# Kernel optimization log

Hardware: AMD Instinct MI355X
Metric: run time of the kernel (lower is better)

## Reference

```python
import jax, jax.numpy as jnp
import numpy as np

N, IN_DIM, HID, Z, HEADS, E = 10000, 128, 128, 64, 4, 320000
NEG_SLOPE = 0.2


def setup_inputs() -> dict:
    key = jax.random.key(0)
    ks = jax.random.split(key, 16)
    s = 0.1
    return {
        "x": jax.random.normal(ks[0], (N, IN_DIM), jnp.float32),
        "edge_index": jax.random.randint(ks[1], (2, E), 0, N, jnp.int64),
        "gcn_w": jax.random.normal(ks[2], (IN_DIM, HID), jnp.float32) * s,
        "gcn_b": jnp.zeros((HID,), jnp.float32),
        "gat_w": jax.random.normal(ks[3], (HID, HEADS * HID), jnp.float32) * s,
        "gat_att_src": jax.random.normal(ks[4], (HEADS, HID), jnp.float32) * s,
        "gat_att_dst": jax.random.normal(ks[5], (HEADS, HID), jnp.float32) * s,
        "gat_b": jnp.zeros((HID,), jnp.float32),
        "mlp_w1": jax.random.normal(ks[6], (HID, HID), jnp.float32) * s,
        "mlp_b1": jnp.zeros((HID,), jnp.float32),
        "mlp_w2": jax.random.normal(ks[7], (HID, HID), jnp.float32) * s,
        "mlp_b2": jnp.zeros((HID,), jnp.float32),
        "mu_w": jax.random.normal(ks[8], (HID, Z), jnp.float32) * s,
        "mu_b": jnp.zeros((Z,), jnp.float32),
        "lv_w": jax.random.normal(ks[9], (HID, Z), jnp.float32) * s,
        "lv_b": jnp.zeros((Z,), jnp.float32),
    }


def _add_self_loops(edge_index, n):
    loop = jnp.arange(n, dtype=edge_index.dtype)
    src = jnp.concatenate([edge_index[0], loop])
    dst = jnp.concatenate([edge_index[1], loop])
    return src, dst


def _gcn(x, edge_index, w, b):
    # PyG GCNConv: add self-loops, symmetric normalization D^-1/2 (A+I) D^-1/2
    n = x.shape[0]
    src, dst = _add_self_loops(edge_index, n)
    deg = jax.ops.segment_sum(jnp.ones_like(dst, dtype=x.dtype), dst, num_segments=n)
    dinv = jax.lax.rsqrt(deg)  # deg >= 1 due to self-loops
    norm = dinv[src] * dinv[dst]  # [E+N]
    h = x @ w  # [N, HID]
    out = jax.ops.segment_sum(h[src] * norm[:, None], dst, num_segments=n)
    return out + b


def _gat(x, edge_index, w, att_src, att_dst, b):
    # PyG GATConv(heads=HEADS, concat=False): average heads, self-loops added
    n = x.shape[0]
    src, dst = _add_self_loops(edge_index, n)
    h = (x @ w).reshape(n, HEADS, HID)  # [N, H, C]
    a_src = jnp.einsum('nhc,hc->nh', h, att_src)  # [N, H]
    a_dst = jnp.einsum('nhc,hc->nh', h, att_dst)
    e = jax.nn.leaky_relu(a_src[src] + a_dst[dst], NEG_SLOPE)  # [E+N, H]
    # segment softmax over incoming edges of each destination node
    emax = jax.ops.segment_max(e, dst, num_segments=n)
    e = jnp.exp(e - emax[dst])
    denom = jax.ops.segment_sum(e, dst, num_segments=n)
    alpha = e / denom[dst]  # [E+N, H]
    out = jax.ops.segment_sum(h[src] * alpha[:, :, None], dst, num_segments=n)  # [N, H, C]
    return out.mean(axis=1) + b


def reference(x, edge_index, gcn_w, gcn_b, gat_w, gat_att_src, gat_att_dst, gat_b,
              mlp_w1, mlp_b1, mlp_w2, mlp_b2, mu_w, mu_b, lv_w, lv_b):
    h = jax.nn.relu(_gcn(x, edge_index, gcn_w, gcn_b))
    h = jax.nn.relu(_gat(h, edge_index, gat_w, gat_att_src, gat_att_dst, gat_b))
    h = jax.nn.relu(h @ mlp_w1 + mlp_b1)
    h = jax.nn.relu(h @ mlp_w2 + mlp_b2)
    mu = h @ mu_w + mu_b
    logvar = h @ lv_w + lv_b
    return (mu, logvar)
```

## Files before the change

kernel.cpp:

```cpp
#include <hip/hip_runtime.h>

#define NN 10000
#define D 128
#define NH 4
#define HD 512
#define ZD 64

__device__ __forceinline__ float lrelu(float x){ return x > 0.0f ? x : 0.2f*x; }

__global__ __launch_bounds__(256) void k_zero_int(int* __restrict__ a, int n){
  int i = blockIdx.x*256 + threadIdx.x;
  if (i < n) a[i] = 0;
}

__global__ __launch_bounds__(256) void k_hist(const int* __restrict__ dst,
                                              int* __restrict__ deg, int E){
  int i = blockIdx.x*256 + threadIdx.x;
  if (i < E) atomicAdd(&deg[dst[i]], 1);
}

__global__ __launch_bounds__(1024) void k_scan(int* __restrict__ deg,
                                               int* __restrict__ ioff,
                                               float* __restrict__ dinv){
  __shared__ int part[1024];
  const int tid = threadIdx.x;
  const int base = tid*10;
  int local[10]; int s = 0;
#pragma unroll
  for (int i=0;i<10;i++){
    int idx = base+i;
    int v = (idx < NN) ? deg[idx] : 0;
    if (idx < NN) dinv[idx] = rsqrtf(1.0f + (float)v);
    local[i] = s; s += v;
  }
  part[tid] = s;
  __syncthreads();
  for (int o=1;o<1024;o<<=1){
    int v = (tid>=o) ? part[tid-o] : 0;
    __syncthreads();
    part[tid] += v;
    __syncthreads();
  }
  int excl = part[tid] - s;
#pragma unroll
  for (int i=0;i<10;i++){
    int idx = base+i;
    if (idx < NN){
      int o = excl + local[i];
      ioff[idx] = o;
      deg[idx]  = o;
    }
  }
  if (tid == 1023) ioff[NN] = part[1023];
}

__global__ __launch_bounds__(256) void k_fill(const int* __restrict__ src,
                                              const int* __restrict__ dst,
                                              int* __restrict__ cur,
                                              int* __restrict__ csr, int E,
                                              float* __restrict__ az){
  int i = blockIdx.x*256 + threadIdx.x;
  if (i < NN*NH*2) az[i] = 0.f;
  if (i >= E) return;
  int pos = atomicAdd(&cur[dst[i]], 1);
  csr[pos] = src[i];
}

__global__ __launch_bounds__(256) void k_gemm(const float* __restrict__ A,
                                              const float* __restrict__ W, int ldw,
                                              const float* __restrict__ bias,
                                              float* __restrict__ C, int ldc,
                                              int nrows, int do_relu){
  __shared__ float As[64][132];
  __shared__ float Ws[128][68];
  const int tid  = threadIdx.x;
  const int row0 = blockIdx.x*64;
  const int col0 = blockIdx.y*64;
#pragma unroll
  for (int i=0;i<8;i++){
    int f  = tid + i*256;
    int r  = f >> 5;
    int k4 = (f & 31) << 2;
    int rr = row0 + r;
    float4 v = make_float4(0.f,0.f,0.f,0.f);
    if (rr < nrows) v = *(const float4*)&A[rr*D + k4];
    *(float4*)&As[r][k4] = v;
  }
#pragma unroll
  for (int i=0;i<8;i++){
    int f  = tid + i*256;
    int k  = f >> 4;
    int c4 = (f & 15) << 2;
    float4 v = *(const float4*)&W[k*ldw + col0 + c4];
    *(float4*)&Ws[k][c4] = v;
  }
  __syncthreads();
  const int tx = tid & 15, ty = tid >> 4;
  float acc[4][4] = {{0.f}};
#pragma unroll 4
  for (int k=0;k<128;k++){
    float4 w = *(const float4*)&Ws[k][tx<<2];
    float wv[4] = {w.x, w.y, w.z, w.w};
    float av[4];
#pragma unroll
    for (int i=0;i<4;i++) av[i] = As[(ty<<2)+i][k];
#pragma unroll
    for (int i=0;i<4;i++)
#pragma unroll
      for (int j=0;j<4;j++) acc[i][j] = fmaf(av[i], wv[j], acc[i][j]);
  }
#pragma unroll
  for (int i=0;i<4;i++){
    int r = row0 + (ty<<2) + i;
    if (r >= nrows) continue;
#pragma unroll
    for (int j=0;j<4;j++){
      int c = col0 + (tx<<2) + j;
      float v = acc[i][j];
      if (bias) v += bias[c];
      if (do_relu) v = fmaxf(v, 0.f);
      C[r*ldc + c] = v;
    }
  }
}

__global__ __launch_bounds__(128) void k_watt(const float* __restrict__ gat_w,
                                              const float* __restrict__ att_src,
                                              const float* __restrict__ att_dst,
                                              float* __restrict__ w_as,
                                              float* __restrict__ w_ad){
  const int h = blockIdx.x;
  const int k = threadIdx.x;
  const float* wrow = &gat_w[k*HD + h*D];
  const float* as   = &att_src[h*D];
  const float* ad   = &att_dst[h*D];
  float s = 0.f, d = 0.f;
#pragma unroll 4
  for (int c=0;c<D;c++){
    float wv = wrow[c];
    s = fmaf(wv, as[c], s);
    d = fmaf(wv, ad[c], d);
  }
  w_as[h*D + k] = s;
  w_ad[h*D + k] = d;
}

__global__ __launch_bounds__(256) void k_gcn_agg(const float* __restrict__ xw,
                                                 const float* __restrict__ dinv,
                                                 const int* __restrict__ ioff,
                                                 const int* __restrict__ csr,
                                                 const float* __restrict__ bias,
                                                 const float* __restrict__ w_as,
                                                 const float* __restrict__ w_ad,
                                                 float* __restrict__ out,
                                                 float* __restrict__ a_src,
                                                 float* __restrict__ a_dst){
  __shared__ float2 snm[4][64];
  const int sub  = blockIdx.x & 7;
  const int ch   = sub >> 2;
  const int g    = blockIdx.x >> 3;
  const int wv   = threadIdx.x >> 6;
  const int lane = threadIdx.x & 63;
  const int w    = g*16 + (sub & 3)*4 + wv;
  const int c    = ch*64 + lane;
  const int beg = ioff[w], end = ioff[w+1];
  float din = dinv[w];
  float ax = xw[w*D + c] * din;
  for (int jb = beg; jb < end; jb += 64){
    int cnt = end - jb; if (cnt > 64) cnt = 64;
    if (lane < cnt){
      int s = csr[jb + lane];
      snm[wv][lane] = make_float2(dinv[s], __int_as_float(s));
    }
    __builtin_amdgcn_wave_barrier();
#pragma unroll 4
    for (int l=0; l<cnt; l++){
      float2 t = snm[wv][l];
      int ss = __float_as_int(t.y);
      ax = fmaf(t.x, xw[ss*D + c], ax);
    }
    __builtin_amdgcn_wave_barrier();
  }
  float val = fmaxf(fmaf(ax, din, bias[c]), 0.f);
  out[w*D + c] = val;
  float ps[NH], pd[NH];
#pragma unroll
  for (int h=0;h<NH;h++){
    ps[h] = val * w_as[h*D + c];
    pd[h] = val * w_ad[h*D + c];
  }
#pragma unroll
  for (int o=32;o>0;o>>=1){
#pragma unroll
    for (int h=0;h<NH;h++){
      ps[h] += __shfl_xor(ps[h], o);
      pd[h] += __shfl_xor(pd[h], o);
    }
  }
  if (lane == 0){
#pragma unroll
    for (int h=0;h<NH;h++){
      atomicAdd(&a_src[w*4 + h], ps[h]);
      atomicAdd(&a_dst[w*4 + h], pd[h]);
    }
  }
}

__global__ __launch_bounds__(256) void k_gat_agg2(const float* __restrict__ h1,
                                                  const float* __restrict__ a_src,
                                                  const float* __restrict__ a_dst,
                                                  const int* __restrict__ ioff,
                                                  const int* __restrict__ csr,
                                                  float* __restrict__ agg){
  __shared__ float4 sal[4][64];
  __shared__ int    ssr[4][64];
  const int sub  = blockIdx.x & 7;
  const int ch   = sub >> 2;
  const int g    = blockIdx.x >> 3;
  const int wv   = threadIdx.x >> 6;
  const int lane = threadIdx.x & 63;
  const int w    = g*16 + (sub & 3)*4 + wv;
  const int c    = ch*64 + lane;
  const int beg = ioff[w], end = ioff[w+1];
  float4 ad  = *(const float4*)&a_dst[w*4];
  float4 asn = *(const float4*)&a_src[w*4];
  float e0 = __expf(lrelu(asn.x + ad.x));
  float e1 = __expf(lrelu(asn.y + ad.y));
  float e2 = __expf(lrelu(asn.z + ad.z));
  float e3 = __expf(lrelu(asn.w + ad.w));
  float hv = h1[w*D + c];
  float o0 = e0*hv, o1 = e1*hv, o2 = e2*hv, o3 = e3*hv;
  float den0=0.f, den1=0.f, den2=0.f, den3=0.f;

  for (int jb = beg; jb < end; jb += 64){
    int cnt = end - jb; if (cnt > 64) cnt = 64;
    if (lane < cnt){
      int s = csr[jb + lane];
      float4 as = *(const float4*)&a_src[s*4];
      float g0 = __expf(lrelu(as.x + ad.x));
      float g1 = __expf(lrelu(as.y + ad.y));
      float g2 = __expf(lrelu(as.z + ad.z));
      float g3 = __expf(lrelu(as.w + ad.w));
      sal[wv][lane] = make_float4(g0,g1,g2,g3);
      ssr[wv][lane] = s;
      den0 += g0; den1 += g1; den2 += g2; den3 += g3;
    }
    __builtin_amdgcn_wave_barrier();
#pragma unroll 4
    for (int l=0; l<cnt; l++){
      float4 b = sal[wv][l];
      float sv = h1[ssr[wv][l]*D + c];
      o0 = fmaf(b.x, sv, o0);
      o1 = fmaf(b.y, sv, o1);
      o2 = fmaf(b.z, sv, o2);
      o3 = fmaf(b.w, sv, o3);
    }
    __builtin_amdgcn_wave_barrier();
  }
#pragma unroll
  for (int o=32; o>0; o>>=1){
    den0 += __shfl_xor(den0, o);
    den1 += __shfl_xor(den1, o);
    den2 += __shfl_xor(den2, o);
    den3 += __shfl_xor(den3, o);
  }
  den0 += e0; den1 += e1; den2 += e2; den3 += e3;
  float* ab = &agg[(size_t)w*HD + c];
  ab[0*D] = o0 * (0.25f/den0);
  ab[1*D] = o1 * (0.25f/den1);
  ab[2*D] = o2 * (0.25f/den2);
  ab[3*D] = o3 * (0.25f/den3);
}

__global__ __launch_bounds__(256) void k_gemm2(const float* __restrict__ agg,
                                               const float* __restrict__ W,
                                               const float* __restrict__ bias,
                                               float* __restrict__ h2){
  __shared__ float As[64][132];
  __shared__ float Ws[128][68];
  const int tid  = threadIdx.x;
  const int row0 = blockIdx.x*64;
  const int col0 = blockIdx.y*64;
  const int tx = tid & 15, ty = tid >> 4;
  float acc[4][4] = {{0.f}};
  for (int h=0; h<NH; h++){
    __syncthreads();
#pragma unroll
    for (int i=0;i<8;i++){
      int f  = tid + i*256;
      int r  = f >> 5;
      int k4 = (f & 31) << 2;
      int rr = row0 + r;
      float4 v = make_float4(0.f,0.f,0.f,0.f);
      if (rr < NN) v = *(const float4*)&agg[(size_t)rr*HD + h*D + k4];
      *(float4*)&As[r][k4] = v;
    }
#pragma unroll
    for (int i=0;i<8;i++){
      int f  = tid + i*256;
      int k  = f >> 4;
      int c4 = (f & 15) << 2;
      *(float4*)&Ws[k][c4] = *(const float4*)&W[k*HD + h*D + col0 + c4];
    }
    __syncthreads();
#pragma unroll 4
    for (int k=0;k<128;k++){
      float4 w = *(const float4*)&Ws[k][tx<<2];
      float wv[4] = {w.x, w.y, w.z, w.w};
      float av[4];
#pragma unroll
      for (int i=0;i<4;i++) av[i] = As[(ty<<2)+i][k];
#pragma unroll
      for (int i=0;i<4;i++)
#pragma unroll
        for (int j=0;j<4;j++) acc[i][j] = fmaf(av[i], wv[j], acc[i][j]);
    }
  }
#pragma unroll
  for (int i=0;i<4;i++){
    int r = row0 + (ty<<2) + i;
    if (r >= NN) continue;
#pragma unroll
    for (int j=0;j<4;j++){
      int col = col0 + (tx<<2) + j;
      h2[r*D + col] = fmaxf(acc[i][j] + bias[col], 0.f);
    }
  }
}

__global__ __launch_bounds__(256) void k_mlp(const float* __restrict__ h2,
                                             const float* __restrict__ w1,
                                             const float* __restrict__ b1,
                                             const float* __restrict__ w2,
                                             const float* __restrict__ b2,
                                             const float* __restrict__ wmu,
                                             const float* __restrict__ bmu,
                                             const float* __restrict__ wlv,
                                             const float* __restrict__ blv,
                                             float* __restrict__ out){
  __shared__ float hA[32][132];
  __shared__ float hB[32][132];
  __shared__ float Ws[128][68];
  const int tid  = threadIdx.x;
  const int row0 = blockIdx.x*32;
  const int tx = tid & 15, ty = tid >> 4;

#pragma unroll
  for (int i=0;i<4;i++){
    int f  = tid + i*256;
    int r  = f >> 5;
    int k4 = (f & 31) << 2;
    int rr = row0 + r;
    float4 v = make_float4(0.f,0.f,0.f,0.f);
    if (rr < NN) v = *(const float4*)&h2[rr*D + k4];
    *(float4*)&hA[r][k4] = v;
  }

  float (*S)[132] = hA;
  float (*T)[132] = hB;
#pragma unroll
  for (int layer=0; layer<2; layer++){
    const float* W  = layer ? w2 : w1;
    const float* bb = layer ? b2 : b1;
    for (int cc=0; cc<2; cc++){
      __syncthreads();
#pragma unroll
      for (int i=0;i<8;i++){
        int f  = tid + i*256;
        int k  = f >> 4;
        int c4 = (f & 15) << 2;
        *(float4*)&Ws[k][c4] = *(const float4*)&W[k*D + cc*64 + c4];
      }
      __syncthreads();
      float acc[2][4] = {{0.f}};
#pragma unroll 4
      for (int k=0;k<128;k++){
        float4 wvv = *(const float4*)&Ws[k][tx<<2];
        float wv[4] = {wvv.x, wvv.y, wvv.z, wvv.w};
        float av[2];
#pragma unroll
        for (int i=0;i<2;i++) av[i] = S[(ty<<1)+i][k];
#pragma unroll
        for (int i=0;i<2;i++)
#pragma unroll
          for (int j=0;j<4;j++) acc[i][j] = fmaf(av[i], wv[j], acc[i][j]);
      }
#pragma unroll
      for (int i=0;i<2;i++)
#pragma unroll
        for (int j=0;j<4;j++){
          int col = cc*64 + (tx<<2) + j;
          T[(ty<<1)+i][col] = fmaxf(acc[i][j] + bb[col], 0.f);
        }
    }
    float (*tmp)[132] = S; S = T; T = tmp;
  }
  for (int cc=0; cc<2; cc++){
    const float* W  = cc ? wlv : wmu;
    const float* bb = cc ? blv : bmu;
    float* ob = out + (size_t)cc*NN*ZD;
    __syncthreads();
#pragma unroll
    for (int i=0;i<8;i++){
      int f  = tid + i*256;
      int k  = f >> 4;
      int c4 = (f & 15) << 2;
      *(float4*)&Ws[k][c4] = *(const float4*)&W[k*ZD + c4];
    }
    __syncthreads();
    float acc[2][4] = {{0.f}};
#pragma unroll 4
    for (int k=0;k<128;k++){
      float4 wvv = *(const float4*)&Ws[k][tx<<2];
      float wv[4] = {wvv.x, wvv.y, wvv.z, wvv.w};
      float av[2];
#pragma unroll
      for (int i=0;i<2;i++) av[i] = S[(ty<<1)+i][k];
#pragma unroll
      for (int i=0;i<2;i++)
#pragma unroll
        for (int j=0;j<4;j++) acc[i][j] = fmaf(av[i], wv[j], acc[i][j]);
    }
#pragma unroll
    for (int i=0;i<2;i++){
      int r = row0 + (ty<<1) + i;
      if (r >= NN) continue;
      float4 v = make_float4(acc[i][0] + bb[(tx<<2)+0],
                             acc[i][1] + bb[(tx<<2)+1],
                             acc[i][2] + bb[(tx<<2)+2],
                             acc[i][3] + bb[(tx<<2)+3]);
      *(float4*)&ob[r*ZD + (tx<<2)] = v;
    }
  }
}

extern "C" void kernel_launch(void* const* d_in, const int* in_sizes, int n_in,
                              void* d_out, int out_size, void* d_ws, size_t ws_size,
                              hipStream_t stream){
  const float* x     = (const float*)d_in[0];
  const int*   ei    = (const int*)d_in[1];
  const float* gcn_w = (const float*)d_in[2];
  const float* gcn_b = (const float*)d_in[3];
  const float* gat_w = (const float*)d_in[4];
  const float* att_s = (const float*)d_in[5];
  const float* att_d = (const float*)d_in[6];
  const float* gat_b = (const float*)d_in[7];
  const float* w1    = (const float*)d_in[8];
  const float* b1    = (const float*)d_in[9];
  const float* w2    = (const float*)d_in[10];
  const float* b2    = (const float*)d_in[11];
  const float* mu_w  = (const float*)d_in[12];
  const float* mu_b  = (const float*)d_in[13];
  const float* lv_w  = (const float*)d_in[14];
  const float* lv_b  = (const float*)d_in[15];
  const int E = in_sizes[1] / 2;
  const int* src = ei;
  const int* dst = ei + E;

  float* ws    = (float*)d_ws;
  float* xw    = ws;
  float* h1    = xw + NN*D;
  float* h2    = h1 + NN*D;
  float* agg   = h2 + NN*D;
  float* dinv  = agg + (size_t)NN*HD;
  float* w_as  = dinv + NN;
  float* w_ad  = w_as + HD;
  float* a_src = w_ad + HD;
  float* a_dst = a_src + NN*NH;
  int*   ioff  = (int*)(a_dst + NN*NH);
  int*   icur  = ioff + NN + 1;
  int*   csr   = icur + NN;

  const int gN = (NN + 255)/256;
  const int gE = (E + 255)/256;
  const int gR = (NN + 63)/64;
  const int gM = (NN + 31)/32;

  k_zero_int<<<gN, 256, 0, stream>>>(icur, NN);
  k_hist<<<gE, 256, 0, stream>>>(dst, icur, E);
  k_scan<<<1, 1024, 0, stream>>>(icur, ioff, dinv);
  k_fill<<<gE, 256, 0, stream>>>(src, dst, icur, csr, E, a_src);

  k_watt<<<NH, 128, 0, stream>>>(gat_w, att_s, att_d, w_as, w_ad);

  k_gemm<<<dim3(gR,2), 256, 0, stream>>>(x, gcn_w, D, nullptr, xw, D, NN, 0);
  k_gcn_agg<<<(NN/16)*8, 256, 0, stream>>>(xw, dinv, ioff, csr, gcn_b,
                                           w_as, w_ad, h1, a_src, a_dst);

  k_gat_agg2<<<(NN/16)*8, 256, 0, stream>>>(h1, a_src, a_dst, ioff, csr, agg);
  k_gemm2<<<dim3(gR,2), 256, 0, stream>>>(agg, gat_w, gat_b, h2);

  k_mlp<<<gM, 256, 0, stream>>>(h2, w1, b1, w2, b2, mu_w, mu_b, lv_w, lv_b,
                                (float*)d_out);
}
```

Baseline: 191.7 us.

## Merge prologue kernels into one launch and fuse GAT projection GEMM into MLP

Combines the zeroing of the degree counters, the attention-weight precompute and the GCN input GEMM into a single multi-role kernel, cutting two launches. The head-summing GAT projection GEMM is folded into the MLP kernel using 32-row tiles, so the h2 intermediate never goes to global memory and one more launch disappears. The trade-off is that the GAT GEMM now runs on smaller tiles with fewer blocks (313) and reloads weights once per block, which lowers per-block data reuse and parallelism for the largest GEMM.

```diff
diff --git a/kernel.cpp b/kernel.cpp
--- a/kernel.cpp
+++ b/kernel.cpp
@@ -7,11 +7,6 @@
 #define ZD 64
 
 __device__ __forceinline__ float lrelu(float x){ return x > 0.0f ? x : 0.2f*x; }
-
-__global__ __launch_bounds__(256) void k_zero_int(int* __restrict__ a, int n){
-  int i = blockIdx.x*256 + threadIdx.x;
-  if (i < n) a[i] = 0;
-}
 
 __global__ __launch_bounds__(256) void k_hist(const int* __restrict__ dst,
                                               int* __restrict__ deg, int E){
@@ -66,83 +61,83 @@
   csr[pos] = src[i];
 }
 
-__global__ __launch_bounds__(256) void k_gemm(const float* __restrict__ A,
-                                              const float* __restrict__ W, int ldw,
-                                              const float* __restrict__ bias,
-                                              float* __restrict__ C, int ldc,
-                                              int nrows, int do_relu){
-  __shared__ float As[64][132];
-  __shared__ float Ws[128][68];
-  const int tid  = threadIdx.x;
-  const int row0 = blockIdx.x*64;
-  const int col0 = blockIdx.y*64;
-#pragma unroll
-  for (int i=0;i<8;i++){
-    int f  = tid + i*256;
-    int r  = f >> 5;
-    int k4 = (f & 31) << 2;
-    int rr = row0 + r;
-    float4 v = make_float4(0.f,0.f,0.f,0.f);
-    if (rr < nrows) v = *(const float4*)&A[rr*D + k4];
-    *(float4*)&As[r][k4] = v;
-  }
-#pragma unroll
-  for (int i=0;i<8;i++){
-    int f  = tid + i*256;
-    int k  = f >> 4;
-    int c4 = (f & 15) << 2;
-    float4 v = *(const float4*)&W[k*ldw + col0 + c4];
-    *(float4*)&Ws[k][c4] = v;
-  }
-  __syncthreads();
-  const int tx = tid & 15, ty = tid >> 4;
-  float acc[4][4] = {{0.f}};
-#pragma unroll 4
-  for (int k=0;k<128;k++){
-    float4 w = *(const float4*)&Ws[k][tx<<2];
-    float wv[4] = {w.x, w.y, w.z, w.w};
-    float av[4];
-#pragma unroll
-    for (int i=0;i<4;i++) av[i] = As[(ty<<2)+i][k];
-#pragma unroll
-    for (int i=0;i<4;i++)
-#pragma unroll
-      for (int j=0;j<4;j++) acc[i][j] = fmaf(av[i], wv[j], acc[i][j]);
-  }
-#pragma unroll
-  for (int i=0;i<4;i++){
-    int r = row0 + (ty<<2) + i;
-    if (r >= nrows) continue;
-#pragma unroll
-    for (int j=0;j<4;j++){
-      int c = col0 + (tx<<2) + j;
-      float v = acc[i][j];
-      if (bias) v += bias[c];
-      if (do_relu) v = fmaxf(v, 0.f);
-      C[r*ldc + c] = v;
-    }
-  }
-}
-
-__global__ __launch_bounds__(128) void k_watt(const float* __restrict__ gat_w,
+__global__ __launch_bounds__(256) void k_mega(const float* __restrict__ x,
+                                              const float* __restrict__ gcn_w,
+                                              float* __restrict__ xw,
+                                              const float* __restrict__ gat_w,
                                               const float* __restrict__ att_src,
                                               const float* __restrict__ att_dst,
                                               float* __restrict__ w_as,
-                                              float* __restrict__ w_ad){
-  const int h = blockIdx.x;
-  const int k = threadIdx.x;
-  const float* wrow = &gat_w[k*HD + h*D];
-  const float* as   = &att_src[h*D];
-  const float* ad   = &att_dst[h*D];
-  float s = 0.f, d = 0.f;
+                                              float* __restrict__ w_ad,
+                                              int* __restrict__ icur){
+  __shared__ float As[64][132];
+  __shared__ float Ws[128][68];
+  const int bx  = blockIdx.x;
+  const int tid = threadIdx.x;
+  if (bx < 314){
+    const int row0 = (bx >> 1)*64;
+    const int col0 = (bx & 1)*64;
+#pragma unroll
+    for (int i=0;i<8;i++){
+      int f  = tid + i*256;
+      int r  = f >> 5;
+      int k4 = (f & 31) << 2;
+      int rr = row0 + r;
+      float4 v = make_float4(0.f,0.f,0.f,0.f);
+      if (rr < NN) v = *(const float4*)&x[rr*D + k4];
+      *(float4*)&As[r][k4] = v;
+    }
+#pragma unroll
+    for (int i=0;i<8;i++){
+      int f  = tid + i*256;
+      int k  = f >> 4;
+      int c4 = (f & 15) << 2;
+      *(float4*)&Ws[k][c4] = *(const float4*)&gcn_w[k*D + col0 + c4];
+    }
+    __syncthreads();
+    const int tx = tid & 15, ty = tid >> 4;
+    float acc[4][4] = {{0.f}};
 #pragma unroll 4
-  for (int c=0;c<D;c++){
-    float wv = wrow[c];
-    s = fmaf(wv, as[c], s);
-    d = fmaf(wv, ad[c], d);
-  }
-  w_as[h*D + k] = s;
-  w_ad[h*D + k] = d;
+    for (int k=0;k<128;k++){
+      float4 w = *(const float4*)&Ws[k][tx<<2];
+      float wv[4] = {w.x, w.y, w.z, w.w};
+      float av[4];
+#pragma unroll
+      for (int i=0;i<4;i++) av[i] = As[(ty<<2)+i][k];
+#pragma unroll
+      for (int i=0;i<4;i++)
+#pragma unroll
+        for (int j=0;j<4;j++) acc[i][j] = fmaf(av[i], wv[j], acc[i][j]);
+    }
+#pragma unroll
+    for (int i=0;i<4;i++){
+      int r = row0 + (ty<<2) + i;
+      if (r >= NN) continue;
+#pragma unroll
+      for (int j=0;j<4;j++)
+        xw[r*D + col0 + (tx<<2) + j] = acc[i][j];
+    }
+  } else if (bx < 318){
+    const int h = bx - 314;
+    const int k = tid;
+    if (k < 128){
+      const float* wrow = &gat_w[k*HD + h*D];
+      const float* as   = &att_src[h*D];
+      const float* ad   = &att_dst[h*D];
+      float s = 0.f, d = 0.f;
+#pragma unroll 4
+      for (int c=0;c<D;c++){
+        float wv = wrow[c];
+        s = fmaf(wv, as[c], s);
+        d = fmaf(wv, ad[c], d);
+      }
+      w_as[h*D + k] = s;
+      w_ad[h*D + k] = d;
+    }
+  } else {
+    int i = (bx - 318)*256 + tid;
+    if (i < NN) icur[i] = 0;
+  }
 }
 
 __global__ __launch_bounds__(256) void k_gcn_agg(const float* __restrict__ xw,
@@ -272,133 +267,131 @@
   ab[3*D] = o3 * (0.25f/den3);
 }
 
-__global__ __launch_bounds__(256) void k_gemm2(const float* __restrict__ agg,
-                                               const float* __restrict__ W,
-                                               const float* __restrict__ bias,
-                                               float* __restrict__ h2){
-  __shared__ float As[64][132];
+#define KLOOP(ACC)                                            \
+  _Pragma("unroll 4")                                         \
+  for (int k=0;k<128;k++){                                    \
+    float4 wvv = *(const float4*)&Ws[k][tx<<2];               \
+    float av0 = S[(ty<<1)+0][k];                              \
+    float av1 = S[(ty<<1)+1][k];                              \
+    ACC[0][0] = fmaf(av0, wvv.x, ACC[0][0]);                  \
+    ACC[0][1] = fmaf(av0, wvv.y, ACC[0][1]);                  \
+    ACC[0][2] = fmaf(av0, wvv.z, ACC[0][2]);                  \
+    ACC[0][3] = fmaf(av0, wvv.w, ACC[0][3]);                  \
+    ACC[1][0] = fmaf(av1, wvv.x, ACC[1][0]);                  \
+    ACC[1][1] = fmaf(av1, wvv.y, ACC[1][1]);                  \
+    ACC[1][2] = fmaf(av1, wvv.z, ACC[1][2]);                  \
+    ACC[1][3] = fmaf(av1, wvv.w, ACC[1][3]);                  \
+  }
+
+__global__ __launch_bounds__(256) void k_gat_mlp(const float* __restrict__ agg,
+                                                 const float* __restrict__ gat_w,
+                                                 const float* __restrict__ gat_b,
+                                                 const float* __restrict__ w1,
+                                                 const float* __restrict__ b1,
+                                                 const float* __restrict__ w2,
+                                                 const float* __restrict__ b2,
+                                                 const float* __restrict__ wmu,
+                                                 const float* __restrict__ bmu,
+                                                 const float* __restrict__ wlv,
+                                                 const float* __restrict__ blv,
+                                                 float* __restrict__ out){
+  __shared__ float S[32][132];
   __shared__ float Ws[128][68];
   const int tid  = threadIdx.x;
-  const int row0 = blockIdx.x*64;
-  const int col0 = blockIdx.y*64;
+  const int row0 = blockIdx.x*32;
   const int tx = tid & 15, ty = tid >> 4;
-  float acc[4][4] = {{0.f}};
+  float accA[2][4] = {{0.f}};
+  float accB[2][4] = {{0.f}};
+
   for (int h=0; h<NH; h++){
     __syncthreads();
 #pragma unroll
-    for (int i=0;i<8;i++){
+    for (int i=0;i<4;i++){
       int f  = tid + i*256;
       int r  = f >> 5;
       int k4 = (f & 31) << 2;
       int rr = row0 + r;
       float4 v = make_float4(0.f,0.f,0.f,0.f);
       if (rr < NN) v = *(const float4*)&agg[(size_t)rr*HD + h*D + k4];
-      *(float4*)&As[r][k4] = v;
-    }
-#pragma unroll
-    for (int i=0;i<8;i++){
-      int f  = tid + i*256;
-      int k  = f >> 4;
-      int c4 = (f & 15) << 2;
-      *(float4*)&Ws[k][c4] = *(const float4*)&W[k*HD + h*D + col0 + c4];
-    }
-    __syncthreads();
-#pragma unroll 4
-    for (int k=0;k<128;k++){
-      float4 w = *(const float4*)&Ws[k][tx<<2];
-      float wv[4] = {w.x, w.y, w.z, w.w};
-      float av[4];
-#pragma unroll
-      for (int i=0;i<4;i++) av[i] = As[(ty<<2)+i][k];
-#pragma unroll
-      for (int i=0;i<4;i++)
-#pragma unroll
-        for (int j=0;j<4;j++) acc[i][j] = fmaf(av[i], wv[j], acc[i][j]);
-    }
-  }
-#pragma unroll
-  for (int i=0;i<4;i++){
-    int r = row0 + (ty<<2) + i;
-    if (r >= NN) continue;
+      *(float4*)&S[r][k4] = v;
+    }
+    __syncthreads();
+#pragma unroll
+    for (int i=0;i<8;i++){
+      int f  = tid + i*256;
+      int k  = f >> 4;
+      int c4 = (f & 15) << 2;
+      *(float4*)&Ws[k][c4] = *(const float4*)&gat_w[k*HD + h*D + 0 + c4];
+    }
+    __syncthreads();
+    KLOOP(accA)
+    __syncthreads();
+#pragma unroll
+    for (int i=0;i<8;i++){
+      int f  = tid + i*256;
+      int k  = f >> 4;
+      int c4 = (f & 15) << 2;
+      *(float4*)&Ws[k][c4] = *(const float4*)&gat_w[k*HD + h*D + 64 + c4];
+    }
+    __syncthreads();
+    KLOOP(accB)
+  }
+  __syncthreads();
+#pragma unroll
+  for (int i=0;i<2;i++)
 #pragma unroll
     for (int j=0;j<4;j++){
-      int col = col0 + (tx<<2) + j;
-      h2[r*D + col] = fmaxf(acc[i][j] + bias[col], 0.f);
-    }
-  }
-}
-
-__global__ __launch_bounds__(256) void k_mlp(const float* __restrict__ h2,
-                                             const float* __restrict__ w1,
-                                             const float* __restrict__ b1,
-                                             const float* __restrict__ w2,
-                                             const float* __restrict__ b2,
-                                             const float* __restrict__ wmu,
-                                             const float* __restrict__ bmu,
-                                             const float* __restrict__ wlv,
-                                             const float* __restrict__ blv,
-                                             float* __restrict__ out){
-  __shared__ float hA[32][132];
-  __shared__ float hB[32][132];
-  __shared__ float Ws[128][68];
-  const int tid  = threadIdx.x;
-  const int row0 = blockIdx.x*32;
-  const int tx = tid & 15, ty = tid >> 4;
-
-#pragma unroll
-  for (int i=0;i<4;i++){
-    int f  = tid + i*256;
-    int r  = f >> 5;
-    int k4 = (f & 31) << 2;
-    int rr = row0 + r;
-    float4 v = make_float4(0.f,0.f,0.f,0.f);
-    if (rr < NN) v = *(const float4*)&h2[rr*D + k4];
-    *(float4*)&hA[r][k4] = v;
-  }
-
-  float (*S)[132] = hA;
-  float (*T)[132] = hB;
-#pragma unroll
+      int c0 = (tx<<2) + j;
+      S[(ty<<1)+i][c0]      = fmaxf(accA[i][j] + gat_b[c0],      0.f);
+      S[(ty<<1)+i][c0 + 64] = fmaxf(accB[i][j] + gat_b[c0 + 64], 0.f);
+    }
+
   for (int layer=0; layer<2; layer++){
     const float* W  = layer ? w2 : w1;
     const float* bb = layer ? b2 : b1;
-    for (int cc=0; cc<2; cc++){
-      __syncthreads();
-#pragma unroll
-      for (int i=0;i<8;i++){
-        int f  = tid + i*256;
-        int k  = f >> 4;
-        int c4 = (f & 15) << 2;
-        *(float4*)&Ws[k][c4] = *(const float4*)&W[k*D + cc*64 + c4];
+#pragma unroll
+    for (int i=0;i<2;i++)
+#pragma unroll
+      for (int j=0;j<4;j++){ accA[i][j] = 0.f; accB[i][j] = 0.f; }
+    __syncthreads();
+#pragma unroll
+    for (int i=0;i<8;i++){
+      int f  = tid + i*256;
+      int k  = f >> 4;
+      int c4 = (f & 15) << 2;
+      *(float4*)&Ws[k][c4] = *(const float4*)&W[k*D + 0 + c4];
+    }
+    __syncthreads();
+    KLOOP(accA)
+    __syncthreads();
+#pragma unroll
+    for (int i=0;i<8;i++){
+      int f  = tid + i*256;
+      int k  = f >> 4;
+      int c4 = (f & 15) << 2;
+      *(float4*)&Ws[k][c4] = *(const float4*)&W[k*D + 64 + c4];
+    }
+    __syncthreads();
+    KLOOP(accB)
+    __syncthreads();
+#pragma unroll
+    for (int i=0;i<2;i++)
+#pragma unroll
+      for (int j=0;j<4;j++){
+        int c0 = (tx<<2) + j;
+        S[(ty<<1)+i][c0]      = fmaxf(accA[i][j] + bb[c0],      0.f);
+        S[(ty<<1)+i][c0 + 64] = fmaxf(accB[i][j] + bb[c0 + 64], 0.f);
       }
-      __syncthreads();
-      float acc[2][4] = {{0.f}};
-#pragma unroll 4
-      for (int k=0;k<128;k++){
-        float4 wvv = *(const float4*)&Ws[k][tx<<2];
-        float wv[4] = {wvv.x, wvv.y, wvv.z, wvv.w};
-        float av[2];
-#pragma unroll
-        for (int i=0;i<2;i++) av[i] = S[(ty<<1)+i][k];
-#pragma unroll
-        for (int i=0;i<2;i++)
-#pragma unroll
-          for (int j=0;j<4;j++) acc[i][j] = fmaf(av[i], wv[j], acc[i][j]);
-      }
-#pragma unroll
-      for (int i=0;i<2;i++)
-#pragma unroll
-        for (int j=0;j<4;j++){
-          int col = cc*64 + (tx<<2) + j;
-          T[(ty<<1)+i][col] = fmaxf(acc[i][j] + bb[col], 0.f);
-        }
-    }
-    float (*tmp)[132] = S; S = T; T = tmp;
-  }
-  for (int cc=0; cc<2; cc++){
-    const float* W  = cc ? wlv : wmu;
-    const float* bb = cc ? blv : bmu;
-    float* ob = out + (size_t)cc*NN*ZD;
+  }
+
+  for (int hd=0; hd<2; hd++){
+    const float* W  = hd ? wlv : wmu;
+    const float* bb = hd ? blv : bmu;
+    float* ob = out + (size_t)hd*NN*ZD;
+#pragma unroll
+    for (int i=0;i<2;i++)
+#pragma unroll
+      for (int j=0;j<4;j++) accA[i][j] = 0.f;
     __syncthreads();
 #pragma unroll
     for (int i=0;i<8;i++){
@@ -408,27 +401,15 @@
       *(float4*)&Ws[k][c4] = *(const float4*)&W[k*ZD + c4];
     }
     __syncthreads();
-    float acc[2][4] = {{0.f}};
-#pragma unroll 4
-    for (int k=0;k<128;k++){
-      float4 wvv = *(const float4*)&Ws[k][tx<<2];
-      float wv[4] = {wvv.x, wvv.y, wvv.z, wvv.w};
-      float av[2];
-#pragma unroll
-      for (int i=0;i<2;i++) av[i] = S[(ty<<1)+i][k];
-#pragma unroll
-      for (int i=0;i<2;i++)
-#pragma unroll
-        for (int j=0;j<4;j++) acc[i][j] = fmaf(av[i], wv[j], acc[i][j]);
-    }
+    KLOOP(accA)
 #pragma unroll
     for (int i=0;i<2;i++){
       int r = row0 + (ty<<1) + i;
       if (r >= NN) continue;
-      float4 v = make_float4(acc[i][0] + bb[(tx<<2)+0],
-                             acc[i][1] + bb[(tx<<2)+1],
-                             acc[i][2] + bb[(tx<<2)+2],
-                             acc[i][3] + bb[(tx<<2)+3]);
+      float4 v = make_float4(accA[i][0] + bb[(tx<<2)+0],
+                             accA[i][1] + bb[(tx<<2)+1],
+                             accA[i][2] + bb[(tx<<2)+2],
+                             accA[i][3] + bb[(tx<<2)+3]);
       *(float4*)&ob[r*ZD + (tx<<2)] = v;
     }
   }
@@ -460,8 +441,7 @@
   float* ws    = (float*)d_ws;
   float* xw    = ws;
   float* h1    = xw + NN*D;
-  float* h2    = h1 + NN*D;
-  float* agg   = h2 + NN*D;
+  float* agg   = h1 + NN*D;
   float* dinv  = agg + (size_t)NN*HD;
   float* w_as  = dinv + NN;
   float* w_ad  = w_as + HD;
@@ -471,25 +451,18 @@
   int*   icur  = ioff + NN + 1;
   int*   csr   = icur + NN;
 
-  const int gN = (NN + 255)/256;
   const int gE = (E + 255)/256;
-  const int gR = (NN + 63)/64;
   const int gM = (NN + 31)/32;
 
-  k_zero_int<<<gN, 256, 0, stream>>>(icur, NN);
+  k_mega<<<358, 256, 0, stream>>>(x, gcn_w, xw, gat_w, att_s, att_d,
+                                  w_as, w_ad, icur);
   k_hist<<<gE, 256, 0, stream>>>(dst, icur, E);
   k_scan<<<1, 1024, 0, stream>>>(icur, ioff, dinv);
   k_fill<<<gE, 256, 0, stream>>>(src, dst, icur, csr, E, a_src);
 
-  k_watt<<<NH, 128, 0, stream>>>(gat_w, att_s, att_d, w_as, w_ad);
-
-  k_gemm<<<dim3(gR,2), 256, 0, stream>>>(x, gcn_w, D, nullptr, xw, D, NN, 0);
   k_gcn_agg<<<(NN/16)*8, 256, 0, stream>>>(xw, dinv, ioff, csr, gcn_b,
                                            w_as, w_ad, h1, a_src, a_dst);
-
   k_gat_agg2<<<(NN/16)*8, 256, 0, stream>>>(h1, a_src, a_dst, ioff, csr, agg);
-  k_gemm2<<<dim3(gR,2), 256, 0, stream>>>(agg, gat_w, gat_b, h2);
-
-  k_mlp<<<gM, 256, 0, stream>>>(h2, w1, b1, w2, b2, mu_w, mu_b, lv_w, lv_b,
-                                (float*)d_out);
-}
+  k_gat_mlp<<<gM, 256, 0, stream>>>(agg, gat_w, gat_b, w1, b1, w2, b2,
+                                    mu_w, mu_b, lv_w, lv_b, (float*)d_out);
+}
```

After: 178.1 us. -7.1%, faster.

## Merge GCN GEMM, attention-weight prep and degree histogram into one kernel; split MLP

Applied to the files above, without the earlier changes.

A single k_mega launch now handles three independent jobs by block index: the x@gcn_w GEMM, the per-head attention-weight projection, and the dst-degree atomic histogram. The separate zero kernel becomes a memset. This removes launches and lets the GEMM and histogram run concurrently. The fused per-row MLP kernel is replaced by two generic 64-row GEMM launches plus a heads kernel with 64x64 tiles, which trades launch count and extra global round-trips for more parallelism and larger register tiles.

```diff
diff --git a/kernel.cpp b/kernel.cpp
--- a/kernel.cpp
+++ b/kernel.cpp
@@ -7,17 +7,6 @@
 #define ZD 64
 
 __device__ __forceinline__ float lrelu(float x){ return x > 0.0f ? x : 0.2f*x; }
-
-__global__ __launch_bounds__(256) void k_zero_int(int* __restrict__ a, int n){
-  int i = blockIdx.x*256 + threadIdx.x;
-  if (i < n) a[i] = 0;
-}
-
-__global__ __launch_bounds__(256) void k_hist(const int* __restrict__ dst,
-                                              int* __restrict__ deg, int E){
-  int i = blockIdx.x*256 + threadIdx.x;
-  if (i < E) atomicAdd(&deg[dst[i]], 1);
-}
 
 __global__ __launch_bounds__(1024) void k_scan(int* __restrict__ deg,
                                                int* __restrict__ ioff,
@@ -66,83 +55,84 @@
   csr[pos] = src[i];
 }
 
-__global__ __launch_bounds__(256) void k_gemm(const float* __restrict__ A,
-                                              const float* __restrict__ W, int ldw,
-                                              const float* __restrict__ bias,
-                                              float* __restrict__ C, int ldc,
-                                              int nrows, int do_relu){
-  __shared__ float As[64][132];
-  __shared__ float Ws[128][68];
-  const int tid  = threadIdx.x;
-  const int row0 = blockIdx.x*64;
-  const int col0 = blockIdx.y*64;
-#pragma unroll
-  for (int i=0;i<8;i++){
-    int f  = tid + i*256;
-    int r  = f >> 5;
-    int k4 = (f & 31) << 2;
-    int rr = row0 + r;
-    float4 v = make_float4(0.f,0.f,0.f,0.f);
-    if (rr < nrows) v = *(const float4*)&A[rr*D + k4];
-    *(float4*)&As[r][k4] = v;
-  }
-#pragma unroll
-  for (int i=0;i<8;i++){
-    int f  = tid + i*256;
-    int k  = f >> 4;
-    int c4 = (f & 15) << 2;
-    float4 v = *(const float4*)&W[k*ldw + col0 + c4];
-    *(float4*)&Ws[k][c4] = v;
-  }
-  __syncthreads();
-  const int tx = tid & 15, ty = tid >> 4;
-  float acc[4][4] = {{0.f}};
-#pragma unroll 4
-  for (int k=0;k<128;k++){
-    float4 w = *(const float4*)&Ws[k][tx<<2];
-    float wv[4] = {w.x, w.y, w.z, w.w};
-    float av[4];
-#pragma unroll
-    for (int i=0;i<4;i++) av[i] = As[(ty<<2)+i][k];
-#pragma unroll
-    for (int i=0;i<4;i++)
-#pragma unroll
-      for (int j=0;j<4;j++) acc[i][j] = fmaf(av[i], wv[j], acc[i][j]);
-  }
-#pragma unroll
-  for (int i=0;i<4;i++){
-    int r = row0 + (ty<<2) + i;
-    if (r >= nrows) continue;
-#pragma unroll
-    for (int j=0;j<4;j++){
-      int c = col0 + (tx<<2) + j;
-      float v = acc[i][j];
-      if (bias) v += bias[c];
-      if (do_relu) v = fmaxf(v, 0.f);
-      C[r*ldc + c] = v;
-    }
-  }
-}
-
-__global__ __launch_bounds__(128) void k_watt(const float* __restrict__ gat_w,
+__global__ __launch_bounds__(256) void k_mega(const float* __restrict__ x,
+                                              const float* __restrict__ gcn_w,
+                                              float* __restrict__ xw,
+                                              const float* __restrict__ gat_w,
                                               const float* __restrict__ att_src,
                                               const float* __restrict__ att_dst,
                                               float* __restrict__ w_as,
-                                              float* __restrict__ w_ad){
-  const int h = blockIdx.x;
-  const int k = threadIdx.x;
-  const float* wrow = &gat_w[k*HD + h*D];
-  const float* as   = &att_src[h*D];
-  const float* ad   = &att_dst[h*D];
-  float s = 0.f, d = 0.f;
-#pragma unroll 4
-  for (int c=0;c<D;c++){
-    float wv = wrow[c];
-    s = fmaf(wv, as[c], s);
-    d = fmaf(wv, ad[c], d);
-  }
-  w_as[h*D + k] = s;
-  w_ad[h*D + k] = d;
+                                              float* __restrict__ w_ad,
+                                              const int* __restrict__ dst,
+                                              int* __restrict__ icur, int E){
+  __shared__ float As[64][132];
+  __shared__ float Ws[128][68];
+  const int bx  = blockIdx.x;
+  const int tid = threadIdx.x;
+  if (bx < 314){
+    const int row0 = (bx >> 1)*64;
+    const int col0 = (bx & 1)*64;
+#pragma unroll
+    for (int i=0;i<8;i++){
+      int f  = tid + i*256;
+      int r  = f >> 5;
+      int k4 = (f & 31) << 2;
+      int rr = row0 + r;
+      float4 v = make_float4(0.f,0.f,0.f,0.f);
+      if (rr < NN) v = *(const float4*)&x[rr*D + k4];
+      *(float4*)&As[r][k4] = v;
+    }
+#pragma unroll
+    for (int i=0;i<8;i++){
+      int f  = tid + i*256;
+      int k  = f >> 4;
+      int c4 = (f & 15) << 2;
+      *(float4*)&Ws[k][c4] = *(const float4*)&gcn_w[k*D + col0 + c4];
+    }
+    __syncthreads();
+    const int tx = tid & 15, ty = tid >> 4;
+    float acc[4][4] = {{0.f}};
+#pragma unroll 4
+    for (int k=0;k<128;k++){
+      float4 w = *(const float4*)&Ws[k][tx<<2];
+      float wv[4] = {w.x, w.y, w.z, w.w};
+      float av[4];
+#pragma unroll
+      for (int i=0;i<4;i++) av[i] = As[(ty<<2)+i][k];
+#pragma unroll
+      for (int i=0;i<4;i++)
+#pragma unroll
+        for (int j=0;j<4;j++) acc[i][j] = fmaf(av[i], wv[j], acc[i][j]);
+    }
+#pragma unroll
+    for (int i=0;i<4;i++){
+      int r = row0 + (ty<<2) + i;
+      if (r >= NN) continue;
+#pragma unroll
+      for (int j=0;j<4;j++)
+        xw[r*D + col0 + (tx<<2) + j] = acc[i][j];
+    }
+  } else if (bx < 318){
+    const int h = bx - 314;
+    const int k = tid;
+    if (k < 128){
+      const float* wrow = &gat_w[k*HD + h*D];
+      const float* as   = &att_src[h*D];
+      const float* ad   = &att_dst[h*D];
+      float s = 0.f, d = 0.f;
+#pragma unroll 4
+      for (int c=0;c<D;c++){
+        float wv = wrow[c];
+        s = fmaf(wv, as[c], s);
+        d = fmaf(wv, ad[c], d);
+      }
+      w_as[h*D + k] = s;
+      w_ad[h*D + k] = d;
+    }
+  } else {
+    int i = (bx - 318)*256 + tid;
+    if (i < E) atomicAdd(&icur[dst[i]], 1);
+  }
 }
 
 __global__ __launch_bounds__(256) void k_gcn_agg(const float* __restrict__ xw,
@@ -272,6 +262,63 @@
   ab[3*D] = o3 * (0.25f/den3);
 }
 
+__global__ __launch_bounds__(256) void k_gemm(const float* __restrict__ A,
+                                              const float* __restrict__ W, int ldw,
+                                              const float* __restrict__ bias,
+                                              float* __restrict__ C, int ldc,
+                                              int nrows, int do_relu){
+  __shared__ float As[64][132];
+  __shared__ float Ws[128][68];
+  const int tid  = threadIdx.x;
+  const int row0 = blockIdx.x*64;
+  const int col0 = blockIdx.y*64;
+#pragma unroll
+  for (int i=0;i<8;i++){
+    int f  = tid + i*256;
+    int r  = f >> 5;
+    int k4 = (f & 31) << 2;
+    int rr = row0 + r;
+    float4 v = make_float4(0.f,0.f,0.f,0.f);
+    if (rr < nrows) v = *(const float4*)&A[rr*D + k4];
+    *(float4*)&As[r][k4] = v;
+  }
+#pragma unroll
+  for (int i=0;i<8;i++){
+    int f  = tid + i*256;
+    int k  = f >> 4;
+    int c4 = (f & 15) << 2;
+    *(float4*)&Ws[k][c4] = *(const float4*)&W[k*ldw + col0 + c4];
+  }
+  __syncthreads();
+  const int tx = tid & 15, ty = tid >> 4;
+  float acc[4][4] = {{0.f}};
+#pragma unroll 4
+  for (int k=0;k<128;k++){
+    float4 w = *(const float4*)&Ws[k][tx<<2];
+    float wv[4] = {w.x, w.y, w.z, w.w};
+    float av[4];
+#pragma unroll
+    for (int i=0;i<4;i++) av[i] = As[(ty<<2)+i][k];
+#pragma unroll
+    for (int i=0;i<4;i++)
+#pragma unroll
+      for (int j=0;j<4;j++) acc[i][j] = fmaf(av[i], wv[j], acc[i][j]);
+  }
+#pragma unroll
+  for (int i=0;i<4;i++){
+    int r = row0 + (ty<<2) + i;
+    if (r >= nrows) continue;
+#pragma unroll
+    for (int j=0;j<4;j++){
+      int c = col0 + (tx<<2) + j;
+      float v = acc[i][j];
+      if (bias) v += bias[c];
+      if (do_relu) v = fmaxf(v, 0.f);
+      C[r*ldc + c] = v;
+    }
+  }
+}
+
 __global__ __launch_bounds__(256) void k_gemm2(const float* __restrict__ agg,
                                                const float* __restrict__ W,
                                                const float* __restrict__ bias,
@@ -328,109 +375,60 @@
   }
 }
 
-__global__ __launch_bounds__(256) void k_mlp(const float* __restrict__ h2,
-                                             const float* __restrict__ w1,
-                                             const float* __restrict__ b1,
-                                             const float* __restrict__ w2,
-                                             const float* __restrict__ b2,
-                                             const float* __restrict__ wmu,
-                                             const float* __restrict__ bmu,
-                                             const float* __restrict__ wlv,
-                                             const float* __restrict__ blv,
-                                             float* __restrict__ out){
-  __shared__ float hA[32][132];
-  __shared__ float hB[32][132];
+__global__ __launch_bounds__(256) void k_heads(const float* __restrict__ h4,
+                                               const float* __restrict__ wmu,
+                                               const float* __restrict__ bmu,
+                                               const float* __restrict__ wlv,
+                                               const float* __restrict__ blv,
+                                               float* __restrict__ out){
+  __shared__ float As[64][132];
   __shared__ float Ws[128][68];
   const int tid  = threadIdx.x;
-  const int row0 = blockIdx.x*32;
-  const int tx = tid & 15, ty = tid >> 4;
-
-#pragma unroll
-  for (int i=0;i<4;i++){
+  const int row0 = blockIdx.x*64;
+  const float* W  = blockIdx.y ? wlv : wmu;
+  const float* bb = blockIdx.y ? blv : bmu;
+  float* ob = out + (size_t)blockIdx.y*NN*ZD;
+#pragma unroll
+  for (int i=0;i<8;i++){
     int f  = tid + i*256;
     int r  = f >> 5;
     int k4 = (f & 31) << 2;
     int rr = row0 + r;
     float4 v = make_float4(0.f,0.f,0.f,0.f);
-    if (rr < NN) v = *(const float4*)&h2[rr*D + k4];
-    *(float4*)&hA[r][k4] = v;
-  }
-
-  float (*S)[132] = hA;
-  float (*T)[132] = hB;
-#pragma unroll
-  for (int layer=0; layer<2; layer++){
-    const float* W  = layer ? w2 : w1;
-    const float* bb = layer ? b2 : b1;
-    for (int cc=0; cc<2; cc++){
-      __syncthreads();
-#pragma unroll
-      for (int i=0;i<8;i++){
-        int f  = tid + i*256;
-        int k  = f >> 4;
-        int c4 = (f & 15) << 2;
-        *(float4*)&Ws[k][c4] = *(const float4*)&W[k*D + cc*64 + c4];
-      }
-      __syncthreads();
-      float acc[2][4] = {{0.f}};
-#pragma unroll 4
-      for (int k=0;k<128;k++){
-        float4 wvv = *(const float4*)&Ws[k][tx<<2];
-        float wv[4] = {wvv.x, wvv.y, wvv.z, wvv.w};
-        float av[2];
-#pragma unroll
-        for (int i=0;i<2;i++) av[i] = S[(ty<<1)+i][k];
-#pragma unroll
-        for (int i=0;i<2;i++)
-#pragma unroll
-          for (int j=0;j<4;j++) acc[i][j] = fmaf(av[i], wv[j], acc[i][j]);
-      }
-#pragma unroll
-      for (int i=0;i<2;i++)
-#pragma unroll
-        for (int j=0;j<4;j++){
-          int col = cc*64 + (tx<<2) + j;
-          T[(ty<<1)+i][col] = fmaxf(acc[i][j] + bb[col], 0.f);
-        }
-    }
-    float (*tmp)[132] = S; S = T; T = tmp;
-  }
-  for (int cc=0; cc<2; cc++){
-    const float* W  = cc ? wlv : wmu;
-    const float* bb = cc ? blv : bmu;
-    float* ob = out + (size_t)cc*NN*ZD;
-    __syncthreads();
-#pragma unroll
-    for (int i=0;i<8;i++){
-      int f  = tid + i*256;
-      int k  = f >> 4;
-      int c4 = (f & 15) << 2;
-      *(float4*)&Ws[k][c4] = *(const float4*)&W[k*ZD + c4];
-    }
-    __syncthreads();
-    float acc[2][4] = {{0.f}};
-#pragma unroll 4
-    for (int k=0;k<128;k++){
-      float4 wvv = *(const float4*)&Ws[k][tx<<2];
-      float wv[4] = {wvv.x, wvv.y, wvv.z, wvv.w};
-      float av[2];
-#pragma unroll
-      for (int i=0;i<2;i++) av[i] = S[(ty<<1)+i][k];
-#pragma unroll
-      for (int i=0;i<2;i++)
-#pragma unroll
-        for (int j=0;j<4;j++) acc[i][j] = fmaf(av[i], wv[j], acc[i][j]);
-    }
-#pragma unroll
-    for (int i=0;i<2;i++){
-      int r = row0 + (ty<<1) + i;
-      if (r >= NN) continue;
-      float4 v = make_float4(acc[i][0] + bb[(tx<<2)+0],
-                             acc[i][1] + bb[(tx<<2)+1],
-                             acc[i][2] + bb[(tx<<2)+2],
-                             acc[i][3] + bb[(tx<<2)+3]);
-      *(float4*)&ob[r*ZD + (tx<<2)] = v;
-    }
+    if (rr < NN) v = *(const float4*)&h4[rr*D + k4];
+    *(float4*)&As[r][k4] = v;
+  }
+#pragma unroll
+  for (int i=0;i<8;i++){
+    int f  = tid + i*256;
+    int k  = f >> 4;
+    int c4 = (f & 15) << 2;
+    *(float4*)&Ws[k][c4] = *(const float4*)&W[k*ZD + c4];
+  }
+  __syncthreads();
+  const int tx = tid & 15, ty = tid >> 4;
+  float acc[4][4] = {{0.f}};
+#pragma unroll 4
+  for (int k=0;k<128;k++){
+    float4 w = *(const float4*)&Ws[k][tx<<2];
+    float wv[4] = {w.x, w.y, w.z, w.w};
+    float av[4];
+#pragma unroll
+    for (int i=0;i<4;i++) av[i] = As[(ty<<2)+i][k];
+#pragma unroll
+    for (int i=0;i<4;i++)
+#pragma unroll
+      for (int j=0;j<4;j++) acc[i][j] = fmaf(av[i], wv[j], acc[i][j]);
+  }
+#pragma unroll
+  for (int i=0;i<4;i++){
+    int r = row0 + (ty<<2) + i;
+    if (r >= NN) continue;
+    float4 v = make_float4(acc[i][0] + bb[(tx<<2)+0],
+                           acc[i][1] + bb[(tx<<2)+1],
+                           acc[i][2] + bb[(tx<<2)+2],
+                           acc[i][3] + bb[(tx<<2)+3]);
+    *(float4*)&ob[r*ZD + (tx<<2)] = v;
   }
 }
 
@@ -460,8 +458,7 @@
   float* ws    = (float*)d_ws;
   float* xw    = ws;
   float* h1    = xw + NN*D;
-  float* h2    = h1 + NN*D;
-  float* agg   = h2 + NN*D;
+  float* agg   = h1 + NN*D;
   float* dinv  = agg + (size_t)NN*HD;
   float* w_as  = dinv + NN;
   float* w_ad  = w_as + HD;
@@ -471,25 +468,23 @@
   int*   icur  = ioff + NN + 1;
   int*   csr   = icur + NN;
 
-  const int gN = (NN + 255)/256;
   const int gE = (E + 255)/256;
   const int gR = (NN + 63)/64;
-  const int gM = (NN + 31)/32;
-
-  k_zero_int<<<gN, 256, 0, stream>>>(icur, NN);
-  k_hist<<<gE, 256, 0, stream>>>(dst, icur, E);
+
+  hipMemsetAsync(icur, 0, NN*sizeof(int), stream);
+
+  k_mega<<<318 + gE, 256, 0, stream>>>(x, gcn_w, xw, gat_w, att_s, att_d,
+                                       w_as, w_ad, dst, icur, E);
   k_scan<<<1, 1024, 0, stream>>>(icur, ioff, dinv);
   k_fill<<<gE, 256, 0, stream>>>(src, dst, icur, csr, E, a_src);
 
-  k_watt<<<NH, 128, 0, stream>>>(gat_w, att_s, att_d, w_as, w_ad);
-
-  k_gemm<<<dim3(gR,2), 256, 0, stream>>>(x, gcn_w, D, nullptr, xw, D, NN, 0);
   k_gcn_agg<<<(NN/16)*8, 256, 0, stream>>>(xw, dinv, ioff, csr, gcn_b,
                                            w_as, w_ad, h1, a_src, a_dst);
-
   k_gat_agg2<<<(NN/16)*8, 256, 0, stream>>>(h1, a_src, a_dst, ioff, csr, agg);
-  k_gemm2<<<dim3(gR,2), 256, 0, stream>>>(agg, gat_w, gat_b, h2);
-
-  k_mlp<<<gM, 256, 0, stream>>>(h2, w1, b1, w2, b2, mu_w, mu_b, lv_w, lv_b,
-                                (float*)d_out);
-}
+
+  k_gemm2<<<dim3(gR,2), 256, 0, stream>>>(agg, gat_w, gat_b, xw);
+  k_gemm <<<dim3(gR,2), 256, 0, stream>>>(xw, w1, D, b1, h1, D, NN, 1);
+  k_gemm <<<dim3(gR,2), 256, 0, stream>>>(h1, w2, D, b2, xw, D, NN, 1);
+  k_heads<<<dim3(gR,2), 256, 0, stream>>>(xw, mu_w, mu_b, lv_w, lv_b,
+                                          (float*)d_out);
+}
```

Measured after the change: 194.9 us. No clear change (+1.6%).
